# Optimization experiments

Measured on AMD Instinct MI355X. Metric: run time of the kernel, lower is better.

## Reference

```python
import jax, jax.numpy as jnp
import numpy as np

NL = 6        # num_layers
V = 512       # pad_vocab_size (d_model)
H = 8         # nhead
HD = V // H   # head dim
DFF = 2048    # dim_feedforward
MAXLEN = 1024 # max distance for relative-position embedding
B = 8
L = 1024
EPS = 1e-5


def _ln(x, g, b):
    m = jnp.mean(x, axis=-1, keepdims=True)
    v = jnp.mean(jnp.square(x - m), axis=-1, keepdims=True)
    return (x - m) * jax.lax.rsqrt(v + EPS) * g + b


def setup_inputs() -> dict:
    key = jax.random.key(0)
    ks = jax.random.split(key, 16)
    s = 0.02
    rn = lambda k, shp: (jax.random.normal(k, shp) * s).astype(jnp.float32)
    return {
        "x": jax.random.uniform(ks[0], (B, L, V), jnp.float32),
        "dist_emb": rn(ks[1], (MAXLEN + 1, H)),
        "in_proj_w": rn(ks[2], (NL, 3 * V, V)),
        "in_proj_b": rn(ks[3], (NL, 3 * V)),
        "out_w": rn(ks[4], (NL, V, V)),
        "out_b": rn(ks[5], (NL, V)),
        "lin1_w": rn(ks[6], (NL, DFF, V)),
        "lin1_b": rn(ks[7], (NL, DFF)),
        "lin2_w": rn(ks[8], (NL, V, DFF)),
        "lin2_b": rn(ks[9], (NL, V)),
        "ln1_g": jnp.ones((NL, V), jnp.float32),
        "ln1_b": jnp.zeros((NL, V), jnp.float32),
        "ln2_g": jnp.ones((NL, V), jnp.float32),
        "ln2_b": jnp.zeros((NL, V), jnp.float32),
        "lnf_g": jnp.ones((V,), jnp.float32),
        "lnf_b": jnp.zeros((V,), jnp.float32),
    }


def _forward(x, dist_emb, in_proj_w, in_proj_b, out_w, out_b,
             lin1_w, lin1_b, lin2_w, lin2_b,
             ln1_g, ln1_b, ln2_g, ln2_b, lnf_g, lnf_b):
    bsz, seqlen, _ = x.shape
    idx = jnp.arange(seqlen)
    dist = jnp.clip(jnp.abs(idx[None, :] - idx[:, None]), 0, MAXLEN)  # (L, L)
    bias = jnp.transpose(dist_emb[dist], (2, 0, 1))[None]  # (1, H, L, L)
    causal = idx[None, :] <= idx[:, None]                   # allow j <= i
    bias = jnp.where(causal[None, None], bias, -jnp.inf)
    kpm = ~jnp.any(x != 0, axis=2)                          # (B, L) key padding
    bias = jnp.where(kpm[:, None, None, :], -jnp.inf, bias)  # (B, H, L, L)

    out = x  # eval mode: dropouts are identity
    scale = 1.0 / np.sqrt(HD)
    for l in range(NL):
        # --- self attention (post-norm TransformerEncoderLayer) ---
        qkv = out @ in_proj_w[l].T + in_proj_b[l]            # (B, L, 3V)
        q, k, v = jnp.split(qkv, 3, axis=-1)
        q = q.reshape(bsz, seqlen, H, HD)
        k = k.reshape(bsz, seqlen, H, HD)
        v = v.reshape(bsz, seqlen, H, HD)
        scores = jnp.einsum('bqhd,bkhd->bhqk', q, k) * scale + bias
        probs = jax.nn.softmax(scores, axis=-1)
        attn = jnp.einsum('bhqk,bkhd->bqhd', probs, v).reshape(bsz, seqlen, V)
        attn = attn @ out_w[l].T + out_b[l]
        out = _ln(out + attn, ln1_g[l], ln1_b[l])
        # --- feed forward (gelu) ---
        h = jax.nn.gelu(out @ lin1_w[l].T + lin1_b[l], approximate=False)
        ff = h @ lin2_w[l].T + lin2_b[l]
        out = _ln(out + ff, ln2_g[l], ln2_b[l])
    return _ln(out, lnf_g, lnf_b)


def reference(x, dist_emb, in_proj_w, in_proj_b, out_w, out_b,
              lin1_w, lin1_b, lin2_w, lin2_b,
              ln1_g, ln1_b, ln2_g, ln2_b, lnf_g, lnf_b):
    return _forward(x, dist_emb, in_proj_w, in_proj_b, out_w, out_b,
                    lin1_w, lin1_b, lin2_w, lin2_b,
                    ln1_g, ln1_b, ln2_g, ln2_b, lnf_g, lnf_b)
```

## Files before the change

kernel.cpp:

```cpp
#include <hip/hip_runtime.h>
#include <hip/hip_bf16.h>
#include <math.h>

#define NL 6
#define V 512
#define H 8
#define HD 64
#define DFF 2048
#define MAXLEN 1024
#define B 8
#define L 1024
#define M (B*L)
#define EPS 1e-5f
#define LOG2E 1.44269504088896f

typedef __hip_bfloat16 bf16;
typedef __attribute__((ext_vector_type(8))) short s8v;
typedef __attribute__((ext_vector_type(4))) float f4v;

__device__ __forceinline__ float b2f(bf16 v){ return __bfloat162float(v); }
__device__ __forceinline__ bf16 f2b(float v){ return __float2bfloat16(v); }
__device__ __forceinline__ unsigned short f2bu(float v){
  return __builtin_bit_cast(unsigned short, __float2bfloat16(v));
}
__device__ __forceinline__ float usf(unsigned short u){
  union{unsigned int i; float f;} c; c.i = ((unsigned int)u)<<16; return c.f;
}

__device__ __forceinline__ float ldin(const void* p, size_t i, int bf){
  if(bf) return b2f(((const bf16*)p)[i]);
  return ((const float*)p)[i];
}

__device__ __forceinline__ void ldin8f(const void* p, size_t e, int bf, float* o){
  if(bf){
    union{uint4 v; unsigned short u[8];} c;
    c.v = *(const uint4*)((const bf16*)p + e);
    #pragma unroll
    for(int i=0;i<8;i++) o[i]=usf(c.u[i]);
  }else{
    const float* f=(const float*)p+e;
    float4 a=*(const float4*)f, b=*(const float4*)(f+4);
    o[0]=a.x;o[1]=a.y;o[2]=a.z;o[3]=a.w;o[4]=b.x;o[5]=b.y;o[6]=b.z;o[7]=b.w;
  }
}

__device__ __forceinline__ uint4 ldw8(const void* W, size_t e, int bf){
  if(bf) return *(const uint4*)((const bf16*)W + e);
  const float* p = (const float*)W + e;
  float4 f0 = *(const float4*)p;
  float4 f1 = *(const float4*)(p+4);
  union { unsigned short u[8]; uint4 v; } r;
  r.u[0]=f2bu(f0.x); r.u[1]=f2bu(f0.y); r.u[2]=f2bu(f0.z); r.u[3]=f2bu(f0.w);
  r.u[4]=f2bu(f1.x); r.u[5]=f2bu(f1.y); r.u[6]=f2bu(f1.z); r.u[7]=f2bu(f1.w);
  return r.v;
}

__device__ __forceinline__ void async16(const bf16* g, unsigned short* l){
  __builtin_amdgcn_global_load_lds((const __attribute__((address_space(1))) void*)g,
                                   (__attribute__((address_space(3))) void*)l, 16, 0, 0);
}

__global__ void k_detect(const void* ones, int* flag){
  unsigned int u = *(const unsigned int*)ones;
  flag[0] = (u == 0x3F803F80u) ? 1 : 0;
  flag[1] = 1;
}

__global__ __launch_bounds__(256) void k_conv(const void* __restrict__ src,
                                              bf16* __restrict__ dst,
                                              const int* __restrict__ flag, int n){
  int bf = *flag;
  int e = (blockIdx.x*256 + threadIdx.x)*8;
  if(e >= n) return;
  if(bf){
    *(uint4*)(dst+e) = *(const uint4*)((const bf16*)src + e);
  }else{
    const float* s = (const float*)src + e;
    float4 a = *(const float4*)s, b2 = *(const float4*)(s+4);
    union{uint4 v; unsigned short u[8];} c;
    c.u[0]=f2bu(a.x); c.u[1]=f2bu(a.y); c.u[2]=f2bu(a.z); c.u[3]=f2bu(a.w);
    c.u[4]=f2bu(b2.x);c.u[5]=f2bu(b2.y);c.u[6]=f2bu(b2.z);c.u[7]=f2bu(b2.w);
    *(uint4*)(dst+e) = c.v;
  }
}

__global__ __launch_bounds__(256) void k_cast_kpm(const void* __restrict__ x,
                                                 const int* __restrict__ flag,
                                                 bf16* __restrict__ cur,
                                                 float* __restrict__ kpm){
  int bf = *flag;
  int row = blockIdx.x; int t = threadIdx.x;
  __shared__ int nz;
  if(t==0) nz = 0;
  __syncthreads();
  int fl = 0;
  for(int e=t; e<V; e+=256){
    float f = ldin(x, (size_t)row*V+e, bf);
    cur[(size_t)row*V+e] = f2b(f);
    if(f != 0.f) fl = 1;
  }
  if(fl) atomicOr(&nz, 1);
  __syncthreads();
  if(t==0) kpm[row] = nz ? 0.f : 1.f;
}

template<int BN, int WM, int WN, int TM, int TN>
__global__ __launch_bounds__(256) void k_gemm(const bf16* __restrict__ A,
                                              const void* __restrict__ W,
                                              const void* __restrict__ bias,
                                              const int* __restrict__ flag,
                                              bf16* __restrict__ C,
                                              int Ndim, int K, int gelu,
                                              size_t w_off, size_t b_off){
  constexpr int TILE = (128+BN)*64;
  constexpr int ES  = BN + 8;
  __shared__ unsigned short lds[2*TILE];
  int bf = *flag;
  int t = threadIdx.x;
  int rb = blockIdx.x*128, cb = blockIdx.y*BN;
  int lane = t & 63, w = t >> 6;
  int wm = w % WM, wn = w / WM;
  int quad = lane >> 4, fid = lane & 15;

  f4v acc[TM][TN];
  #pragma unroll
  for(int i=0;i<TM;i++)
    #pragma unroll
    for(int j=0;j<TN;j++){ f4v z = {0.f,0.f,0.f,0.f}; acc[i][j] = z; }

  auto stage = [&](int kt, int bsel){
    unsigned short* Ad = lds + bsel*TILE;
    unsigned short* Bd = Ad + 128*64;
    int k0 = kt*64;
    #pragma unroll
    for(int i=0;i<4;i++){
      int r = w*32 + i*8 + (lane>>3);
      const bf16* g = A + (size_t)(rb+r)*K + k0 + (((lane&7)^(r&7))<<3);
      async16(g, Ad + (w*32 + i*8)*64);
    }
    if(bf){
      #pragma unroll
      for(int i=0;i<BN/32;i++){
        int r = w*(BN/4) + i*8 + (lane>>3);
        const bf16* g = (const bf16*)W + w_off + (size_t)(cb+r)*K + k0 + (((lane&7)^(r&7))<<3);
        async16(g, Bd + (w*(BN/4) + i*8)*64);
      }
    }else{
      const int tpr = 256/BN;
      int sr = t/tpr;
      int sc0 = (t%tpr)*(64/tpr);
      #pragma unroll
      for(int c=0;c<64/tpr;c+=8){
        uint4 d = ldw8(W, w_off + (size_t)(cb+sr)*K + k0 + sc0 + c, 0);
        int chunk = (sc0+c)>>3;
        *(uint4*)&Bd[sr*64 + ((chunk^(sr&7))<<3)] = d;
      }
    }
  };

  int KT = K/64;
  stage(0, 0);
  __syncthreads();
  int cur = 0;
  for(int kt=0;kt<KT;kt++){
    if(kt+1<KT) stage(kt+1, cur^1);
    unsigned short* As = lds + cur*TILE;
    unsigned short* Bs = As + 128*64;
    #pragma unroll
    for(int h=0;h<2;h++){
      s8v av[TM], bv[TN];
      #pragma unroll
      for(int tm=0;tm<TM;tm++){
        int r = wm*(TM*16) + tm*16 + fid;
        av[tm] = *(const s8v*)&As[r*64 + (((h*4+quad)^(r&7))<<3)];
      }
      #pragma unroll
      for(int tn=0;tn<TN;tn++){
        int c = wn*(TN*16) + tn*16 + fid;
        bv[tn] = *(const s8v*)&Bs[c*64 + (((h*4+quad)^(c&7))<<3)];
      }
      #pragma unroll
      for(int tm=0;tm<TM;tm++)
        #pragma unroll
        for(int tn=0;tn<TN;tn++)
          acc[tm][tn] = __builtin_amdgcn_mfma_f32_16x16x32_bf16(av[tm], bv[tn], acc[tm][tn], 0,0,0);
    }
    __syncthreads();
    cur ^= 1;
  }

  float bvv[TN];
  #pragma unroll
  for(int tn=0;tn<TN;tn++)
    bvv[tn] = ldin(bias, b_off + cb + wn*(TN*16) + tn*16 + fid, bf);
  unsigned short* E = lds;
  #pragma unroll
  for(int tn=0;tn<TN;tn++){
    int col = wn*(TN*16) + tn*16 + fid;
    #pragma unroll
    for(int tm=0;tm<TM;tm++)
      #pragma unroll
      for(int rg=0; rg<4; rg++){
        int row = wm*(TM*16) + tm*16 + quad*4 + rg;
        float v = acc[tm][tn][rg] + bvv[tn];
        if(gelu){
          float u = v*(0.7978845608f + 0.0356774081f*v*v);
          float e = __builtin_amdgcn_exp2f(u*(2.f*LOG2E));
          v = v - v*__builtin_amdgcn_rcpf(e + 1.f);
        }
        E[row*ES + col] = f2bu(v);
      }
  }
  __syncthreads();
  int row = t>>1, c0 = (t&1)*(BN/2);
  bf16* cp = C + (size_t)(rb+row)*Ndim + cb + c0;
  #pragma unroll
  for(int c=0;c<BN/2;c+=8)
    *(uint4*)(cp + c) = *(const uint4*)&E[row*ES + c0 + c];
}

__global__ __launch_bounds__(512) void k_attn(const bf16* __restrict__ qkv,
                                              const void* __restrict__ dist_emb,
                                              const int* __restrict__ flag,
                                              const float* __restrict__ kpm,
                                              bf16* __restrict__ out){
  int bf = *flag;
  int t = threadIdx.x;
  int bh = blockIdx.x; int b = bh>>3, h = bh&7;
  int p = blockIdx.y;
  int wg = t>>8, tg = t&255;
  int w = tg>>6, lane = tg&63, quad = lane>>4, fid = lane&15;
  int ww = t>>6;

  __shared__ unsigned short Ks[2][64][70];
  __shared__ unsigned short Vt[2][64][70];
  __shared__ unsigned short PsRaw[8*16*70];
  __shared__ float distc[L];
  __shared__ float kflagS[2][64];
  __shared__ float mlX[4][16][2];

  int qt0 = p, qt1 = 15-p;
  int c0 = qt0+1, c1 = qt1+1;
  int I0 = (c0+1)>>1, IT = I0 + ((c1+1)>>1);

  int dmax = c1*64;
  for(int i=t;i<dmax;i+=512) distc[i] = ldin(dist_emb,(size_t)i*H+h,bf) * LOG2E;

  int r  = tg>>2, dc = (tg&3)*16;
  int d0 = (tg&15)*4, jj = (tg>>4)*4;
  uint4 kr0, kr1; uint2 vb[4]; float kf;

  auto tileJ = [&](int i)->int{
    if(i < 0 || i >= IT) return -1;
    if(i < I0){ int jt = 2*i + wg; return (jt < c0) ? jt : -1; }
    int jt = 2*(i-I0) + wg; return (jt < c1) ? jt : -1;
  };

  auto loadrg = [&](int j0){
    size_t kbase = (size_t)(b*L+j0+r)*(3*V) + h*HD + dc;
    kr0 = *(const uint4*)(qkv + kbase + V);
    kr1 = *(const uint4*)(qkv + kbase + V + 8);
    #pragma unroll
    for(int k2=0;k2<4;k2++)
      vb[k2] = *(const uint2*)(qkv + (size_t)(b*L+j0+jj+k2)*(3*V) + 2*V + h*HD + d0);
    kf = (tg < 64) ? kpm[b*L + j0 + tg] : 0.f;
  };

  auto store_tile = [&](){
    *(uint4*)&Ks[wg][r][dc]   = kr0;
    *(uint4*)&Ks[wg][r][dc+8] = kr1;
    const unsigned short* v0 = (const unsigned short*)&vb[0];
    const unsigned short* v1 = (const unsigned short*)&vb[1];
    const unsigned short* v2 = (const unsigned short*)&vb[2];
    const unsigned short* v3 = (const unsigned short*)&vb[3];
    #pragma unroll
    for(int i2=0;i2<4;i2++){
      unsigned short o[4] = {v0[i2], v1[i2], v2[i2], v3[i2]};
      *(uint2*)&Vt[wg][d0+i2][jj] = *(uint2*)o;
    }
    if(tg < 64) kflagS[wg][tg] = kf;
  };

  s8v aq0, aq1;
  auto loadQ = [&](int rbase){
    int qrow = rbase + w*16 + fid;
    const bf16* qp = qkv + (size_t)(b*L+qrow)*(3*V) + h*HD;
    aq0 = *(const s8v*)(qp + quad*8);
    aq1 = *(const s8v*)(qp + 32 + quad*8);
  };

  float mrow = -1e30f, lrow = 0.f;
  f4v Oc[4];
  #pragma unroll
  for(int q2=0;q2<4;q2++){ f4v z={0.f,0.f,0.f,0.f}; Oc[q2]=z; }

  float* Om = (float*)PsRaw;
  auto mergeOut = [&](int rbase){
    if(wg==1){
      #pragma unroll
      for(int nt=0;nt<4;nt++)
        #pragma unroll
        for(int rg=0;rg<4;rg++)
          Om[(w*16 + quad*4+rg)*68 + nt*16+fid] = Oc[nt][rg];
      if(quad==0){ mlX[w][fid][0] = mrow; mlX[w][fid][1] = lrow; }
    }
    __syncthreads();
    if(wg==0){
      #pragma unroll
      for(int rg=0;rg<4;rg++){
        int qr = quad*4 + rg;
        float mB = mlX[w][qr][0], lB = mlX[w][qr][1];
        float mA = __shfl(mrow, (lane&48)|qr);
        float lA = __shfl(lrow, (lane&48)|qr);
        float mM = fmaxf(mA, mB);
        float msub = (mM <= -1e29f) ? 0.f : mM;
        float sA = __builtin_amdgcn_exp2f(mA - msub);
        float sB = __builtin_amdgcn_exp2f(mB - msub);
        float lm = lA*sA + lB*sB;
        float inv = (lm > 0.f) ? 1.f/lm : 0.f;
        int row = rbase + w*16 + qr;
        #pragma unroll
        for(int nt=0;nt<4;nt++){
          float ov = Oc[nt][rg]*sA + Om[(w*16 + qr)*68 + nt*16+fid]*sB;
          out[(size_t)(b*L+row)*V + h*HD + nt*16 + fid] = f2b(ov*inv);
        }
      }
    }
  };

  int rb = qt0*64;
  loadQ(rb);

  { int j = tileJ(0); if(j>=0){ loadrg(j*64); store_tile(); }
    j = tileJ(1); if(j>=0) loadrg(j*64); }
  __syncthreads();

  for(int it=0; it<IT; it++){
    int ph = (it >= I0);
    int qt = ph ? qt1 : qt0;
    int jt = tileJ(it);
    if(jt >= 0){
      int j0 = jt*64;
      f4v Sc[4];
      #pragma unroll
      for(int nt=0;nt<4;nt++){ f4v z={0.f,0.f,0.f,0.f}; Sc[nt]=z; }
      __builtin_amdgcn_s_setprio(1);
      #pragma unroll
      for(int nt=0;nt<4;nt++){
        s8v bk0 = *(const s8v*)&Ks[wg][nt*16+fid][quad*8];
        s8v bk1 = *(const s8v*)&Ks[wg][nt*16+fid][32+quad*8];
        Sc[nt] = __builtin_amdgcn_mfma_f32_16x16x32_bf16(bk0, aq0, Sc[nt], 0,0,0);
        Sc[nt] = __builtin_amdgcn_mfma_f32_16x16x32_bf16(bk1, aq1, Sc[nt], 0,0,0);
      }
      __builtin_amdgcn_s_setprio(0);

      int diag = (jt == qt);
      int row_q = rb + w*16 + fid;
      float sv[4][4];
      #pragma unroll
      for(int nt=0;nt<4;nt++){
        #pragma unroll
        for(int rg=0;rg<4;rg++){
          int kk = nt*16 + quad*4 + rg;
          int col_j = j0 + kk;
          int kmask = (kflagS[wg][kk] != 0.f);
          int masked = kmask | (diag & (col_j > row_q));
          float bias = masked ? 0.f : distc[row_q - col_j];
          sv[nt][rg] = masked ? -1e30f : fmaf(Sc[nt][rg], 0.125f*LOG2E, bias);
        }
      }

      float t0 = fmaxf(fmaxf(sv[0][0],sv[0][1]),fmaxf(sv[0][2],sv[0][3]));
      float t1 = fmaxf(fmaxf(sv[1][0],sv[1][1]),fmaxf(sv[1][2],sv[1][3]));
      float t2 = fmaxf(fmaxf(sv[2][0],sv[2][1]),fmaxf(sv[2][2],sv[2][3]));
      float t3 = fmaxf(fmaxf(sv[3][0],sv[3][1]),fmaxf(sv[3][2],sv[3][3]));
      float tmax = fmaxf(fmaxf(t0,t1),fmaxf(t2,t3));
      tmax = fmaxf(tmax, __shfl_xor(tmax, 16));
      tmax = fmaxf(tmax, __shfl_xor(tmax, 32));
      float nm1 = fmaxf(mrow, tmax);
      int growany = __any(nm1 > mrow);
      float msub = (nm1 <= -1e29f) ? 0.f : nm1;
      float alpha = growany ? __builtin_amdgcn_exp2f(mrow - msub) : 1.f;
      mrow = nm1;
      float ps = 0.f;
      #pragma unroll
      for(int nt=0;nt<4;nt++)
        #pragma unroll
        for(int rg=0;rg<4;rg++){
          float pv = __builtin_amdgcn_exp2f(sv[nt][rg]-msub);
          sv[nt][rg] = pv;
          ps += pv;
        }
      ps += __shfl_xor(ps, 16);
      ps += __shfl_xor(ps, 32);
      lrow = lrow*alpha + ps;
      if(growany){
        #pragma unroll
        for(int rg=0;rg<4;rg++){
          float ar = __shfl(alpha, (lane&48)|(quad*4+rg));
          #pragma unroll
          for(int nt=0;nt<4;nt++) Oc[nt][rg] *= ar;
        }
      }

      unsigned short* Ps = PsRaw + ww*16*70;
      #pragma unroll
      for(int nt=0;nt<4;nt++)
        #pragma unroll
        for(int rg=0;rg<4;rg++)
          Ps[fid*70 + nt*16 + quad*4 + rg] = f2bu(sv[nt][rg]);
      s8v ap0 = *(const s8v*)&Ps[fid*70 + quad*8];
      s8v ap1 = *(const s8v*)&Ps[fid*70 + 32 + quad*8];
      __builtin_amdgcn_s_setprio(1);
      #pragma unroll
      for(int nt=0;nt<4;nt++){
        s8v bv0 = *(const s8v*)&Vt[wg][nt*16+fid][quad*8];
        s8v bv1 = *(const s8v*)&Vt[wg][nt*16+fid][32+quad*8];
        Oc[nt] = __builtin_amdgcn_mfma_f32_16x16x32_bf16(ap0, bv0, Oc[nt], 0,0,0);
        Oc[nt] = __builtin_amdgcn_mfma_f32_16x16x32_bf16(ap1, bv1, Oc[nt], 0,0,0);
      }
      __builtin_amdgcn_s_setprio(0);
    }
    __syncthreads();

    if(it == I0-1){
      mergeOut(rb);
      rb = qt1*64;
      loadQ(rb);
      mrow = -1e30f; lrow = 0.f;
      #pragma unroll
      for(int q2=0;q2<4;q2++){ f4v z={0.f,0.f,0.f,0.f}; Oc[q2]=z; }
    }

    { int jn = tileJ(it+1); if(jn>=0) store_tile();
      int j2 = tileJ(it+2); if(j2>=0) loadrg(j2*64); }
    __syncthreads();
  }
  mergeOut(rb);
}

__global__ __launch_bounds__(256) void k_ln(const bf16* __restrict__ a,
                                            const bf16* __restrict__ r,
                                            const void* __restrict__ g,
                                            const void* __restrict__ be,
                                            const int* __restrict__ flag,
                                            void* __restrict__ outp,
                                            int use_r, int final_out,
                                            size_t gb_off){
  int bf = *flag;
  int t = threadIdx.x, w = t>>6, lane = t&63;
  int row = blockIdx.x*4 + w;
  size_t o = (size_t)row*V + lane*8;
  union{uint4 v; unsigned short u[8];} ua;
  ua.v = *(const uint4*)(a + o);
  float v[8];
  #pragma unroll
  for(int i=0;i<8;i++) v[i] = usf(ua.u[i]);
  if(use_r){
    union{uint4 v; unsigned short u[8];} ur;
    ur.v = *(const uint4*)(r + o);
    #pragma unroll
    for(int i=0;i<8;i++) v[i] += usf(ur.u[i]);
  }
  float s=0.f, q=0.f;
  #pragma unroll
  for(int i=0;i<8;i++){ s += v[i]; q += v[i]*v[i]; }
  #pragma unroll
  for(int m=1;m<64;m<<=1){ s += __shfl_xor(s, m); q += __shfl_xor(q, m); }
  float mean = s * (1.f/V);
  float var  = q * (1.f/V) - mean*mean;
  float rstd = 1.f / sqrtf(var + EPS);
  float gv[8], bv[8], ov[8];
  ldin8f(g,  gb_off + lane*8, bf, gv);
  ldin8f(be, gb_off + lane*8, bf, bv);
  #pragma unroll
  for(int i=0;i<8;i++) ov[i] = (v[i]-mean)*rstd*gv[i] + bv[i];
  if(final_out && !bf){
    float* op = (float*)outp + o;
    *(float4*)op     = make_float4(ov[0],ov[1],ov[2],ov[3]);
    *(float4*)(op+4) = make_float4(ov[4],ov[5],ov[6],ov[7]);
  }else{
    union{uint4 v; unsigned short u[8];} c;
    #pragma unroll
    for(int i=0;i<8;i++) c.u[i] = f2bu(ov[i]);
    *(uint4*)((bf16*)outp + o) = c.v;
  }
}

extern "C" void kernel_launch(void* const* d_in, const int* in_sizes, int n_in,
                              void* d_out, int out_size, void* d_ws, size_t ws_size,
                              hipStream_t stream){
  const void* x         = d_in[0];
  const void* dist_emb  = d_in[1];
  const void* in_proj_w = d_in[2];
  const void* in_proj_b = d_in[3];
  const void* out_w     = d_in[4];
  const void* out_b     = d_in[5];
  const void* lin1_w    = d_in[6];
  const void* lin1_b    = d_in[7];
  const void* lin2_w    = d_in[8];
  const void* lin2_b    = d_in[9];
  const void* ln1_g     = d_in[10];
  const void* ln1_bb    = d_in[11];
  const void* ln2_g     = d_in[12];
  const void* ln2_bb    = d_in[13];
  const void* lnf_g     = d_in[14];
  const void* lnf_bb    = d_in[15];

  int*   flag    = (int*)d_ws;
  int*   flagOne = flag + 1;
  float* kpm  = (float*)((char*)d_ws + 256);
  bf16*  cur  = (bf16*)(kpm + M);
  bf16*  big  = cur + (size_t)M*V;
  bf16*  attn = big + (size_t)M*(3*V);
  bf16*  proj = big + (size_t)M*DFF;
  char*  base_end = (char*)(proj + (size_t)M*V);

  const size_t S_ipw = (size_t)NL*3*V*V, S_ow = (size_t)NL*V*V;
  const size_t S_l1w = (size_t)NL*DFF*V, S_l2w = (size_t)NL*V*DFF;
  const size_t S_ipb = (size_t)NL*3*V, S_ob = (size_t)NL*V;
  const size_t S_l1b = (size_t)NL*DFF, S_l2b = (size_t)NL*V;
  const size_t SW = S_ipw + S_ow + S_l1w + S_l2w;
  const size_t SB = S_ipb + S_ob + S_l1b + S_l2b;
  size_t need = (size_t)(base_end - (char*)d_ws) + (SW + SB)*sizeof(bf16);
  int conv = (ws_size >= need);

  bf16* w_ip = (bf16*)base_end;
  bf16* w_o  = w_ip + S_ipw;
  bf16* w_l1 = w_o  + S_ow;
  bf16* w_l2 = w_l1 + S_l1w;
  bf16* b_ip = w_l2 + S_l2w;
  bf16* b_o  = b_ip + S_ipb;
  bf16* b_l1 = b_o  + S_ob;
  bf16* b_l2 = b_l1 + S_l1b;

  k_detect<<<1, 1, 0, stream>>>(lnf_g, flag);
  k_cast_kpm<<<M, 256, 0, stream>>>(x, flag, cur, kpm);

  const int* gflag = conv ? flagOne : flag;
  const void* g_ipw = conv ? (const void*)w_ip : in_proj_w;
  const void* g_ow  = conv ? (const void*)w_o  : out_w;
  const void* g_l1w = conv ? (const void*)w_l1 : lin1_w;
  const void* g_l2w = conv ? (const void*)w_l2 : lin2_w;
  const void* g_ipb = conv ? (const void*)b_ip : in_proj_b;
  const void* g_ob  = conv ? (const void*)b_o  : out_b;
  const void* g_l1b = conv ? (const void*)b_l1 : lin1_b;
  const void* g_l2b = conv ? (const void*)b_l2 : lin2_b;

  if(conv){
    auto cv = [&](const void* s, bf16* d, size_t n){
      k_conv<<<(unsigned)((n/8 + 255)/256), 256, 0, stream>>>(s, d, flag, (int)n);
    };
    cv(in_proj_w, w_ip, S_ipw);  cv(out_w, w_o, S_ow);
    cv(lin1_w, w_l1, S_l1w);     cv(lin2_w, w_l2, S_l2w);
    cv(in_proj_b, b_ip, S_ipb);  cv(out_b, b_o, S_ob);
    cv(lin1_b, b_l1, S_l1b);     cv(lin2_b, b_l2, S_l2b);
  }

  for(int l=0;l<NL;l++){
    k_gemm<128,2,2,4,4><<<dim3(M/128, (3*V)/128), 256, 0, stream>>>(
        cur, g_ipw, g_ipb, gflag, big, 3*V, V, 0,
        (size_t)l*3*V*V, (size_t)l*3*V);
    k_attn<<<dim3(B*H, 8), 512, 0, stream>>>(big, dist_emb, flag, kpm, attn);
    k_gemm<64,4,1,2,4><<<dim3(M/128, V/64), 256, 0, stream>>>(
        attn, g_ow, g_ob, gflag, proj, V, V, 0,
        (size_t)l*V*V, (size_t)l*V);
    k_ln<<<M/4, 256, 0, stream>>>(cur, proj, ln1_g, ln1_bb, flag, cur, 1, 0, (size_t)l*V);
    k_gemm<128,2,2,4,4><<<dim3(M/128, DFF/128), 256, 0, stream>>>(
        cur, g_l1w, g_l1b, gflag, big, DFF, V, 1,
        (size_t)l*DFF*V, (size_t)l*DFF);
    k_gemm<64,4,1,2,4><<<dim3(M/128, V/64), 256, 0, stream>>>(
        big, g_l2w, g_l2b, gflag, proj, V, DFF, 0,
        (size_t)l*V*DFF, (size_t)l*V);
    k_ln<<<M/4, 256, 0, stream>>>(cur, proj, ln2_g, ln2_bb, flag, cur, 1, 0, (size_t)l*V);
  }
  k_ln<<<M/4, 256, 0, stream>>>(cur, cur, lnf_g, lnf_bb, flag, d_out, 0, 1, 0);
}
```

Before: 1.216 ms.

## Triple-buffer GEMM K-loop with vmcnt waits, shrink QKV/FFN1 tiles, pack P stores

The GEMM main loop now uses three LDS stages and prefetches two K-tiles ahead. Full __syncthreads calls are replaced by explicit s_waitcnt vmcnt on the async path plus a raw s_barrier, so loads stay in flight across iterations. The QKV and FFN1 GEMMs switch from 128x128 to 128x64 tiles, which doubles the block count but lowers per-block reuse. The attention kernel also packs bf16 P values into 32-bit LDS stores. The larger LDS footprint and the hand-set wait counts add occupancy and correctness risk.

New measurement: 1.229 ms. About the same (+1.1%).

```diff
diff --git a/kernel.cpp b/kernel.cpp
--- a/kernel.cpp
+++ b/kernel.cpp
@@ -115,7 +115,7 @@
                                               size_t w_off, size_t b_off){
   constexpr int TILE = (128+BN)*64;
   constexpr int ES  = BN + 8;
-  __shared__ unsigned short lds[2*TILE];
+  __shared__ unsigned short lds[3*TILE];
   int bf = *flag;
   int t = threadIdx.x;
   int rb = blockIdx.x*128, cb = blockIdx.y*BN;
@@ -161,11 +161,13 @@
 
   int KT = K/64;
   stage(0, 0);
-  __syncthreads();
-  int cur = 0;
+  stage(1, 1);
+  if(bf){ asm volatile("s_waitcnt vmcnt(6)" ::: "memory"); }
+  else  { asm volatile("s_waitcnt vmcnt(0) lgkmcnt(0)" ::: "memory"); }
+  __builtin_amdgcn_s_barrier();
+  __builtin_amdgcn_sched_barrier(0);
   for(int kt=0;kt<KT;kt++){
-    if(kt+1<KT) stage(kt+1, cur^1);
-    unsigned short* As = lds + cur*TILE;
+    unsigned short* As = lds + (kt%3)*TILE;
     unsigned short* Bs = As + 128*64;
     #pragma unroll
     for(int h=0;h<2;h++){
@@ -186,9 +188,17 @@
         for(int tn=0;tn<TN;tn++)
           acc[tm][tn] = __builtin_amdgcn_mfma_f32_16x16x32_bf16(av[tm], bv[tn], acc[tm][tn], 0,0,0);
     }
-    __syncthreads();
-    cur ^= 1;
-  }
+    if(kt+2<KT) stage(kt+2, (kt+2)%3);
+    if(bf){
+      if(kt+2<KT)      { asm volatile("s_waitcnt vmcnt(6)" ::: "memory"); }
+      else if(kt+1<KT) { asm volatile("s_waitcnt vmcnt(0)" ::: "memory"); }
+    }else{
+      asm volatile("s_waitcnt vmcnt(0) lgkmcnt(0)" ::: "memory");
+    }
+    __builtin_amdgcn_s_barrier();
+    __builtin_amdgcn_sched_barrier(0);
+  }
+  __syncthreads();
 
   float bvv[TN];
   #pragma unroll
@@ -406,10 +416,12 @@
 
       unsigned short* Ps = PsRaw + ww*16*70;
       #pragma unroll
-      for(int nt=0;nt<4;nt++)
-        #pragma unroll
-        for(int rg=0;rg<4;rg++)
-          Ps[fid*70 + nt*16 + quad*4 + rg] = f2bu(sv[nt][rg]);
+      for(int nt=0;nt<4;nt++){
+        unsigned int u0 = (unsigned int)f2bu(sv[nt][0]) | ((unsigned int)f2bu(sv[nt][1])<<16);
+        unsigned int u1 = (unsigned int)f2bu(sv[nt][2]) | ((unsigned int)f2bu(sv[nt][3])<<16);
+        unsigned int* dp = (unsigned int*)&Ps[fid*70 + nt*16 + quad*4];
+        dp[0] = u0; dp[1] = u1;
+      }
       s8v ap0 = *(const s8v*)&Ps[fid*70 + quad*8];
       s8v ap1 = *(const s8v*)&Ps[fid*70 + 32 + quad*8];
       __builtin_amdgcn_s_setprio(1);
@@ -559,7 +571,7 @@
   }
 
   for(int l=0;l<NL;l++){
-    k_gemm<128,2,2,4,4><<<dim3(M/128, (3*V)/128), 256, 0, stream>>>(
+    k_gemm<64,4,1,2,4><<<dim3(M/128, (3*V)/64), 256, 0, stream>>>(
         cur, g_ipw, g_ipb, gflag, big, 3*V, V, 0,
         (size_t)l*3*V*V, (size_t)l*3*V);
     k_attn<<<dim3(B*H, 8), 512, 0, stream>>>(big, dist_emb, flag, kpm, attn);
@@ -567,7 +579,7 @@
         attn, g_ow, g_ob, gflag, proj, V, V, 0,
         (size_t)l*V*V, (size_t)l*V);
     k_ln<<<M/4, 256, 0, stream>>>(cur, proj, ln1_g, ln1_bb, flag, cur, 1, 0, (size_t)l*V);
-    k_gemm<128,2,2,4,4><<<dim3(M/128, DFF/128), 256, 0, stream>>>(
+    k_gemm<64,4,1,2,4><<<dim3(M/128, DFF/64), 256, 0, stream>>>(
         cur, g_l1w, g_l1b, gflag, big, DFF, V, 1,
         (size_t)l*DFF*V, (size_t)l*DFF);
     k_gemm<64,4,1,2,4><<<dim3(M/128, V/64), 256, 0, stream>>>(
```

## Add 256x256-tile GEMM kernel for QKV and FFN1 projections; pack P stores

Applied to the files above, without the earlier changes.

Introduces a new 512-thread GEMM kernel with 256x256 output tiles, double-buffered async LDS staging and a four-pass epilogue. It is used for the QKV and first FFN projections to raise arithmetic intensity per tile and cut global/LDS traffic per MFMA. Separately, attention probability stores to LDS are packed into 32-bit writes instead of 16-bit ones. The larger tiles use 128 KB of LDS per block and launch far fewer blocks (e.g. 192 for QKV), which may underfill the GPU.

After: 1.266 ms. 1.04x slower.

```diff
diff --git a/kernel.cpp b/kernel.cpp
--- a/kernel.cpp
+++ b/kernel.cpp
@@ -220,6 +220,124 @@
     *(uint4*)(cp + c) = *(const uint4*)&E[row*ES + c0 + c];
 }
 
+__global__ __launch_bounds__(512, 2) void k_gemm_big(const bf16* __restrict__ A,
+                                                     const void* __restrict__ W,
+                                                     const void* __restrict__ bias,
+                                                     const int* __restrict__ flag,
+                                                     bf16* __restrict__ C,
+                                                     int Ndim, int K, int gelu,
+                                                     size_t w_off, size_t b_off){
+  constexpr int TILE = 512*64;
+  constexpr int ES = 264;
+  __shared__ unsigned short lds[2*TILE];
+  int bf = *flag;
+  int t = threadIdx.x;
+  int rb = blockIdx.x*256, cb = blockIdx.y*256;
+  int lane = t & 63, w = t >> 6;
+  int wm = w & 3, wn = w >> 2;
+  int quad = lane >> 4, fid = lane & 15;
+
+  f4v acc[4][8];
+  #pragma unroll
+  for(int i=0;i<4;i++)
+    #pragma unroll
+    for(int j=0;j<8;j++){ f4v z = {0.f,0.f,0.f,0.f}; acc[i][j] = z; }
+
+  auto stage = [&](int kt, int bsel){
+    unsigned short* Ad = lds + bsel*TILE;
+    unsigned short* Bd = Ad + 256*64;
+    int k0 = kt*64;
+    #pragma unroll
+    for(int i=0;i<4;i++){
+      int r = w*32 + i*8 + (lane>>3);
+      const bf16* g = A + (size_t)(rb+r)*K + k0 + (((lane&7)^(r&7))<<3);
+      async16(g, Ad + (w*32 + i*8)*64);
+    }
+    if(bf){
+      #pragma unroll
+      for(int i=0;i<4;i++){
+        int r = w*32 + i*8 + (lane>>3);
+        const bf16* g = (const bf16*)W + w_off + (size_t)(cb+r)*K + k0 + (((lane&7)^(r&7))<<3);
+        async16(g, Bd + (w*32 + i*8)*64);
+      }
+    }else{
+      int sr = t>>1, sc0 = (t&1)*32;
+      #pragma unroll
+      for(int c=0;c<32;c+=8){
+        uint4 d = ldw8(W, w_off + (size_t)(cb+sr)*K + k0 + sc0 + c, 0);
+        int chunk = (sc0+c)>>3;
+        *(uint4*)&Bd[sr*64 + ((chunk^(sr&7))<<3)] = d;
+      }
+    }
+  };
+
+  int KT = K/64;
+  stage(0, 0);
+  __syncthreads();
+  int cur = 0;
+  for(int kt=0;kt<KT;kt++){
+    if(kt+1<KT) stage(kt+1, cur^1);
+    unsigned short* As = lds + cur*TILE;
+    unsigned short* Bs = As + 256*64;
+    #pragma unroll
+    for(int h=0;h<2;h++){
+      s8v av[4], bv[8];
+      #pragma unroll
+      for(int tm=0;tm<4;tm++){
+        int r = wm*64 + tm*16 + fid;
+        av[tm] = *(const s8v*)&As[r*64 + (((h*4+quad)^(r&7))<<3)];
+      }
+      #pragma unroll
+      for(int tn=0;tn<8;tn++){
+        int c = wn*128 + tn*16 + fid;
+        bv[tn] = *(const s8v*)&Bs[c*64 + (((h*4+quad)^(c&7))<<3)];
+      }
+      #pragma unroll
+      for(int tm=0;tm<4;tm++)
+        #pragma unroll
+        for(int tn=0;tn<8;tn++)
+          acc[tm][tn] = __builtin_amdgcn_mfma_f32_16x16x32_bf16(av[tm], bv[tn], acc[tm][tn], 0,0,0);
+    }
+    __syncthreads();
+    cur ^= 1;
+  }
+
+  float bvv[8];
+  #pragma unroll
+  for(int tn=0;tn<8;tn++)
+    bvv[tn] = ldin(bias, b_off + cb + wn*128 + tn*16 + fid, bf);
+  unsigned short* E = lds;
+  #pragma unroll
+  for(int pass=0; pass<4; pass++){
+    if(wm == pass){
+      #pragma unroll
+      for(int tn=0;tn<8;tn++){
+        int col = wn*128 + tn*16 + fid;
+        #pragma unroll
+        for(int tm=0;tm<4;tm++)
+          #pragma unroll
+          for(int rg=0; rg<4; rg++){
+            int lr = tm*16 + quad*4 + rg;
+            float v = acc[tm][tn][rg] + bvv[tn];
+            if(gelu){
+              float u = v*(0.7978845608f + 0.0356774081f*v*v);
+              float e = __builtin_amdgcn_exp2f(u*(2.f*LOG2E));
+              v = v - v*__builtin_amdgcn_rcpf(e + 1.f);
+            }
+            E[lr*ES + col] = f2bu(v);
+          }
+      }
+    }
+    __syncthreads();
+    int row = t>>3, c0 = (t&7)*32;
+    bf16* cp = C + (size_t)(rb + pass*64 + row)*Ndim + cb + c0;
+    #pragma unroll
+    for(int c=0;c<32;c+=8)
+      *(uint4*)(cp + c) = *(const uint4*)&E[row*ES + c0 + c];
+    __syncthreads();
+  }
+}
+
 __global__ __launch_bounds__(512) void k_attn(const bf16* __restrict__ qkv,
                                               const void* __restrict__ dist_emb,
                                               const int* __restrict__ flag,
@@ -406,10 +524,12 @@
 
       unsigned short* Ps = PsRaw + ww*16*70;
       #pragma unroll
-      for(int nt=0;nt<4;nt++)
-        #pragma unroll
-        for(int rg=0;rg<4;rg++)
-          Ps[fid*70 + nt*16 + quad*4 + rg] = f2bu(sv[nt][rg]);
+      for(int nt=0;nt<4;nt++){
+        unsigned int u0 = (unsigned int)f2bu(sv[nt][0]) | ((unsigned int)f2bu(sv[nt][1])<<16);
+        unsigned int u1 = (unsigned int)f2bu(sv[nt][2]) | ((unsigned int)f2bu(sv[nt][3])<<16);
+        unsigned int* dp = (unsigned int*)&Ps[fid*70 + nt*16 + quad*4];
+        dp[0] = u0; dp[1] = u1;
+      }
       s8v ap0 = *(const s8v*)&Ps[fid*70 + quad*8];
       s8v ap1 = *(const s8v*)&Ps[fid*70 + 32 + quad*8];
       __builtin_amdgcn_s_setprio(1);
@@ -559,7 +679,7 @@
   }
 
   for(int l=0;l<NL;l++){
-    k_gemm<128,2,2,4,4><<<dim3(M/128, (3*V)/128), 256, 0, stream>>>(
+    k_gemm_big<<<dim3(M/256, (3*V)/256), 512, 0, stream>>>(
         cur, g_ipw, g_ipb, gflag, big, 3*V, V, 0,
         (size_t)l*3*V*V, (size_t)l*3*V);
     k_attn<<<dim3(B*H, 8), 512, 0, stream>>>(big, dist_emb, flag, kpm, attn);
@@ -567,7 +687,7 @@
         attn, g_ow, g_ob, gflag, proj, V, V, 0,
         (size_t)l*V*V, (size_t)l*V);
     k_ln<<<M/4, 256, 0, stream>>>(cur, proj, ln1_g, ln1_bb, flag, cur, 1, 0, (size_t)l*V);
-    k_gemm<128,2,2,4,4><<<dim3(M/128, DFF/128), 256, 0, stream>>>(
+    k_gemm_big<<<dim3(M/256, DFF/256), 512, 0, stream>>>(
         cur, g_l1w, g_l1b, gflag, big, DFF, V, 1,
         (size_t)l*DFF*V, (size_t)l*DFF);
     k_gemm<64,4,1,2,4><<<dim3(M/128, V/64), 256, 0, stream>>>(
```
